# Optimization experiments

Hardware: AMD Instinct MI355X
Metric: run time of the kernel (lower is better)

Reference implementation:

```python
import jax, jax.numpy as jnp
import numpy as np
from jax import lax

V, E, H, MLP, NCLS = 50000, 100, 100, 300, 3
B, T, C = 256, 128, 255


def _lstm_dir(x, Wih, Whh, bih, bhh, reverse):
    # x: [T, B, E]; PyTorch gate order i, f, g, o
    Bsz = x.shape[1]
    h0 = jnp.zeros((Bsz, H), x.dtype)
    c0 = jnp.zeros((Bsz, H), x.dtype)

    def step(carry, xt):
        h, c = carry
        gates = xt @ Wih.T + h @ Whh.T + (bih + bhh)  # [B, 4H]
        i, f, g, o = jnp.split(gates, 4, axis=-1)
        c = jax.nn.sigmoid(f) * c + jax.nn.sigmoid(i) * jnp.tanh(g)
        h = jax.nn.sigmoid(o) * jnp.tanh(c)
        return (h, c), h

    _, hs = lax.scan(step, (h0, c0), x, reverse=reverse)
    return hs  # [T, B, H]


def setup_inputs() -> dict:
    key = jax.random.key(0)
    ks = jax.random.split(key, 16)
    s_e = 1.0 / np.sqrt(H)
    inp = {
        "x": jax.random.randint(ks[0], (B, T), 0, V),
        "paths": jax.random.randint(ks[1], (B, C, 3), 0, T),
        "emb": jax.random.normal(ks[2], (V, E), jnp.float32),
        "Wih_f": jax.random.uniform(ks[3], (4 * H, E), jnp.float32, -s_e, s_e),
        "Whh_f": jax.random.uniform(ks[4], (4 * H, H), jnp.float32, -s_e, s_e),
        "bih_f": jax.random.uniform(ks[5], (4 * H,), jnp.float32, -s_e, s_e),
        "bhh_f": jax.random.uniform(ks[6], (4 * H,), jnp.float32, -s_e, s_e),
        "Wih_b": jax.random.uniform(ks[7], (4 * H, E), jnp.float32, -s_e, s_e),
        "Whh_b": jax.random.uniform(ks[8], (4 * H, H), jnp.float32, -s_e, s_e),
        "bih_b": jax.random.uniform(ks[9], (4 * H,), jnp.float32, -s_e, s_e),
        "bhh_b": jax.random.uniform(ks[10], (4 * H,), jnp.float32, -s_e, s_e),
        "W1": jax.random.normal(ks[11], (6 * H, MLP), jnp.float32) * 0.05,
        "b1": jnp.zeros((MLP,), jnp.float32),
        "W2": jax.random.normal(ks[12], (MLP, NCLS), jnp.float32) * 0.05,
        "b2": jnp.zeros((NCLS,), jnp.float32),
    }
    return inp


def reference(x, paths, emb, Wih_f, Whh_f, bih_f, bhh_f, Wih_b, Whh_b, bih_b, bhh_b, W1, b1, W2, b2):
    # embedding lookup (dropout is eval-mode identity)
    xe = emb[x]                      # [B, T, E]
    xe = jnp.transpose(xe, (1, 0, 2))  # [T, B, E] (seq-major like packed LSTM)
    hf = _lstm_dir(xe, Wih_f, Whh_f, bih_f, bhh_f, reverse=False)
    hb = _lstm_dir(xe, Wih_b, Whh_b, bih_b, bhh_b, reverse=True)
    h = jnp.concatenate([hf, hb], axis=-1)        # [T, B, 2H]
    hbt = jnp.transpose(h, (1, 0, 2))             # [B, T, 2H]
    # gather 3 positions per configuration; index -1 -> zero vector
    idx = jnp.clip(paths, 0, T - 1)               # [B, C, 3]
    g = hbt[jnp.arange(hbt.shape[0])[:, None, None], idx]  # [B, C, 3, 2H]
    g = jnp.where((paths >= 0)[..., None], g, 0.0)
    mlp_in = g.reshape(-1, 6 * H)                 # [B*C, 600]
    hdn = jnp.tanh(mlp_in @ W1 + b1)
    return jax.nn.softmax(hdn @ W2 + b2, axis=-1)  # [B*C, 3]
```

## Files before the change

### kernel.cpp

```cpp
#include <hip/hip_runtime.h>

typedef unsigned short u16;
typedef short short8 __attribute__((ext_vector_type(8)));
typedef float f32x4 __attribute__((ext_vector_type(4)));

__device__ __forceinline__ u16 f2b(float x){
  union{float f; unsigned u;} v; v.f = x;
  unsigned r = (v.u + 0x7FFFu + ((v.u >> 16) & 1u)) >> 16;
  return (u16)r;
}
__device__ __forceinline__ float b2f(u16 h){
  union{unsigned u; float f;} v; v.u = ((unsigned)h) << 16; return v.f;
}
__device__ __forceinline__ float sigm(float x){ return 1.0f/(1.0f + __expf(-x)); }
__device__ __forceinline__ float tanh_f(float x){ return 1.0f - 2.0f/(1.0f + __expf(2.0f*x)); }

__global__ void prep_kernel(const int* __restrict__ x, const float* __restrict__ emb,
   const float* __restrict__ Wih_f, const float* __restrict__ Whh_f,
   const float* __restrict__ bih_f, const float* __restrict__ bhh_f,
   const float* __restrict__ Wih_b, const float* __restrict__ Whh_b,
   const float* __restrict__ bih_b, const float* __restrict__ bhh_b,
   const float* __restrict__ W1,
   u16* __restrict__ xe, u16* __restrict__ wc, float* __restrict__ biasC,
   float* __restrict__ whhT, u16* __restrict__ w1b, u16* __restrict__ hbt)
{
  int id = blockIdx.x*256 + threadIdx.x;
  const int N0 = 32768*128;
  const int N1 = 832*128;
  const int N2 = 800;
  const int N3 = 80000;
  const int N4 = 672*320;
  const int N5 = 32768*24;
  if (id < N0){
    int p = id >> 7, k = id & 127;
    float v = 0.f;
    if (k < 100) v = emb[x[p]*100 + k];
    xe[id] = f2b(v);
    return;
  }
  id -= N0;
  if (id < N1){
    int n = id >> 7, k = id & 127;
    float v = 0.f;
    if (k < 100){
      if (n < 400) v = Wih_f[n*100+k];
      else if (n < 800) v = Wih_b[(n-400)*100+k];
    }
    wc[id] = f2b(v);
    return;
  }
  id -= N1;
  if (id < N2){
    biasC[id] = (id < 400) ? (bih_f[id]+bhh_f[id]) : (bih_b[id-400]+bhh_b[id-400]);
    return;
  }
  id -= N2;
  if (id < N3){
    int d = id / 40000; int rem = id - d*40000; int k = rem / 400; int j = rem - k*400;
    const float* W = d ? Whh_b : Whh_f;
    whhT[id] = W[j*100 + k];
    return;
  }
  id -= N3;
  if (id < N4){
    int k = id / 320; int n = id - k*320;
    int seg = k / 224; int wwk = k - seg*224;
    float v = 0.f;
    if (n < 300 && wwk < 200) v = W1[(seg*200 + wwk)*300 + n];
    w1b[n*672 + k] = f2b(v);
    return;
  }
  id -= N4;
  if (id < N5){
    int p = id / 24; int k = id - p*24;
    hbt[p*224 + 200 + k] = 0;
  }
}

__global__ __launch_bounds__(256) void gemm1_kernel(const u16* __restrict__ xe,
    const u16* __restrict__ wc, const float* __restrict__ biasC, u16* __restrict__ inp)
{
  __shared__ __align__(16) u16 As[64*136];
  __shared__ __align__(16) u16 Bs[64*136];
  const int m0 = blockIdx.x*64, n0 = blockIdx.y*64;
  const int tid = threadIdx.x;
  #pragma unroll
  for (int i=0;i<4;i++){
    int f = i*256 + tid;
    int row = f >> 4, c8 = f & 15;
    *(uint4*)&As[row*136 + c8*8] = *(const uint4*)&xe[(m0+row)*128 + c8*8];
    *(uint4*)&Bs[row*136 + c8*8] = *(const uint4*)&wc[(n0+row)*128 + c8*8];
  }
  __syncthreads();
  const int w = tid >> 6, lane = tid & 63, col = lane & 15, quad = lane >> 4;
  f32x4 acc[4];
  #pragma unroll
  for (int nt=0;nt<4;nt++) acc[nt] = (f32x4){0.f,0.f,0.f,0.f};
  #pragma unroll
  for (int kc=0;kc<4;kc++){
    short8 af = *(const short8*)&As[(w*16+col)*136 + kc*32 + quad*8];
    #pragma unroll
    for (int nt=0;nt<4;nt++){
      short8 bfrag = *(const short8*)&Bs[(nt*16+col)*136 + kc*32 + quad*8];
      acc[nt] = __builtin_amdgcn_mfma_f32_16x16x32_bf16(af, bfrag, acc[nt], 0, 0, 0);
    }
  }
  #pragma unroll
  for (int nt=0;nt<4;nt++){
    int n = n0 + nt*16 + col;
    if (n < 800){
      float bs = biasC[n];
      int dir = (n >= 400) ? 1 : 0;
      int j = n - dir*400;
      #pragma unroll
      for (int r=0;r<4;r++){
        int m = m0 + w*16 + quad*4 + r;
        inp[(dir*32768 + m)*400 + j] = f2b(acc[nt][r] + bs);
      }
    }
  }
}

__global__ __launch_bounds__(448, 4) void lstm_kernel(const u16* __restrict__ inp,
    const float* __restrict__ whhT, u16* __restrict__ hbt)
{
  const int cid = blockIdx.x;
  const int b = cid & 255, dir = cid >> 8;
  const int jj = threadIdx.x;
  __shared__ __align__(16) float hs[104];
  __shared__ float act[400];
  float whh[100];
  if (jj < 400){
    const float* wp = whhT + dir*40000 + jj;
    #pragma unroll
    for (int k=0;k<100;k++) whh[k] = wp[k*400];
  }
  if (jj < 104) hs[jj] = 0.f;
  float c = 0.f;
  const u16* ip = inp + (dir*32768 + b*128)*400;
  u16* hp = hbt + b*128*224;
  __syncthreads();
  for (int step=0; step<128; step++){
    int t = dir ? (127-step) : step;
    if (jj < 400){
      float pre = b2f(ip[t*400 + jj]);
      const float4* h4 = (const float4*)hs;
      float a0=0.f,a1=0.f,a2=0.f,a3=0.f;
      #pragma unroll
      for (int kk=0;kk<25;kk++){
        float4 hv = h4[kk];
        a0 = fmaf(whh[4*kk+0], hv.x, a0);
        a1 = fmaf(whh[4*kk+1], hv.y, a1);
        a2 = fmaf(whh[4*kk+2], hv.z, a2);
        a3 = fmaf(whh[4*kk+3], hv.w, a3);
      }
      float xg = pre + ((a0+a1)+(a2+a3));
      act[jj] = (jj >= 200 && jj < 300) ? tanh_f(xg) : sigm(xg);
    }
    __syncthreads();
    if (jj < 100){
      float ig = act[jj], fg = act[100+jj], gg = act[200+jj], og = act[300+jj];
      c = fg*c + ig*gg;
      float hk = og * tanh_f(c);
      hs[jj] = hk;
      hp[t*224 + dir*100 + jj] = f2b(hk);
    }
    __syncthreads();
  }
}

__global__ __launch_bounds__(512) void mlp_kernel(const u16* __restrict__ hbt,
    const u16* __restrict__ w1b, const int* __restrict__ paths,
    const float* __restrict__ b1, const float* __restrict__ W2,
    const float* __restrict__ b2, float* __restrict__ out)
{
  __shared__ __align__(16) u16 As[128*40];
  __shared__ __align__(16) u16 Bs[320*40];
  const int m0 = blockIdx.x*128;
  const int tid = threadIdx.x;
  const int arow = tid >> 2, ac8 = tid & 3;
  const int am = m0 + arow;
  const int ab = am / 255;
  const int w = tid >> 6, lane = tid & 63, col = lane & 15, quad = lane >> 4;
  f32x4 acc[20];
  #pragma unroll
  for (int nt=0;nt<20;nt++) acc[nt] = (f32x4){0.f,0.f,0.f,0.f};
  for (int kc=0;kc<21;kc++){
    __syncthreads();
    for (int f = tid; f < 1280; f += 512){
      int br = f >> 2, bc = f & 3;
      *(uint4*)&Bs[br*40 + bc*8] = *(const uint4*)&w1b[br*672 + kc*32 + bc*8];
    }
    int seg = (kc >= 14) ? 2 : (kc >= 7 ? 1 : 0);
    int ko = kc - seg*7;
    int it = paths[am*3 + seg];
    uint4 v = make_uint4(0u,0u,0u,0u);
    if (it >= 0){
      int t = it > 127 ? 127 : it;
      v = *(const uint4*)&hbt[(ab*128 + t)*224 + ko*32 + ac8*8];
    }
    *(uint4*)&As[arow*40 + ac8*8] = v;
    __syncthreads();
    short8 af = *(const short8*)&As[(w*16+col)*40 + quad*8];
    #pragma unroll
    for (int nt=0;nt<20;nt++){
      short8 bfrag = *(const short8*)&Bs[(nt*16+col)*40 + quad*8];
      acc[nt] = __builtin_amdgcn_mfma_f32_16x16x32_bf16(af, bfrag, acc[nt], 0, 0, 0);
    }
  }
  float pz[4][3];
  #pragma unroll
  for (int r=0;r<4;r++){ pz[r][0]=0.f; pz[r][1]=0.f; pz[r][2]=0.f; }
  #pragma unroll
  for (int nt=0;nt<20;nt++){
    int n = nt*16 + col;
    if (n < 300){
      float bb = b1[n];
      float w20 = W2[n*3+0], w21 = W2[n*3+1], w22 = W2[n*3+2];
      #pragma unroll
      for (int r=0;r<4;r++){
        float hdn = tanh_f(acc[nt][r] + bb);
        pz[r][0] = fmaf(hdn, w20, pz[r][0]);
        pz[r][1] = fmaf(hdn, w21, pz[r][1]);
        pz[r][2] = fmaf(hdn, w22, pz[r][2]);
      }
    }
  }
  #pragma unroll
  for (int off=1; off<16; off<<=1){
    #pragma unroll
    for (int r=0;r<4;r++){
      pz[r][0] += __shfl_xor(pz[r][0], off, 64);
      pz[r][1] += __shfl_xor(pz[r][1], off, 64);
      pz[r][2] += __shfl_xor(pz[r][2], off, 64);
    }
  }
  float c0 = b2[0], c1 = b2[1], c2 = b2[2];
  #pragma unroll
  for (int r=0;r<4;r++){
    float z0 = pz[r][0]+c0, z1 = pz[r][1]+c1, z2 = pz[r][2]+c2;
    float mx = fmaxf(z0, fmaxf(z1, z2));
    float e0 = __expf(z0-mx), e1 = __expf(z1-mx), e2 = __expf(z2-mx);
    float inv = 1.0f/(e0+e1+e2);
    if (col < 3){
      float pv = (col==0 ? e0 : (col==1 ? e1 : e2)) * inv;
      out[(m0 + w*16 + quad*4 + r)*3 + col] = pv;
    }
  }
}

extern "C" void kernel_launch(void* const* d_in, const int* in_sizes, int n_in,
                              void* d_out, int out_size, void* d_ws, size_t ws_size,
                              hipStream_t stream)
{
  const int*   x     = (const int*)  d_in[0];
  const int*   paths = (const int*)  d_in[1];
  const float* emb   = (const float*)d_in[2];
  const float* Wih_f = (const float*)d_in[3];
  const float* Whh_f = (const float*)d_in[4];
  const float* bih_f = (const float*)d_in[5];
  const float* bhh_f = (const float*)d_in[6];
  const float* Wih_b = (const float*)d_in[7];
  const float* Whh_b = (const float*)d_in[8];
  const float* bih_b = (const float*)d_in[9];
  const float* bhh_b = (const float*)d_in[10];
  const float* W1    = (const float*)d_in[11];
  const float* b1    = (const float*)d_in[12];
  const float* W2    = (const float*)d_in[13];
  const float* b2    = (const float*)d_in[14];
  float* out = (float*)d_out;

  char* ws = (char*)d_ws;
  u16*   xe    = (u16*)  (ws + 0);
  u16*   wc    = (u16*)  (ws + 8388608);
  float* biasC = (float*)(ws + 8601600);
  float* whhT  = (float*)(ws + 8604800);
  u16*   w1b   = (u16*)  (ws + 8924800);
  u16*   inp   = (u16*)  (ws + 9354880);
  u16*   hbt   = (u16*)  (ws + 61783680);

  const int prep_total = 32768*128 + 832*128 + 800 + 80000 + 672*320 + 32768*24;
  prep_kernel<<<(prep_total + 255)/256, 256, 0, stream>>>(
      x, emb, Wih_f, Whh_f, bih_f, bhh_f, Wih_b, Whh_b, bih_b, bhh_b, W1,
      xe, wc, biasC, whhT, w1b, hbt);
  gemm1_kernel<<<dim3(512, 13), 256, 0, stream>>>(xe, wc, biasC, inp);
  lstm_kernel<<<512, 448, 0, stream>>>(inp, whhT, hbt);
  mlp_kernel<<<510, 512, 0, stream>>>(hbt, w1b, paths, b1, W2, b2, out);
}
```

Before: 364.4 us.

## Rewrite LSTM recurrence in inline assembly with interleaved gates and swizzle exchange

Gate columns are permuted so each hidden unit's four gates sit in adjacent lanes, letting the recurrence exchange gate values via ds_swizzle within a quad instead of through shared memory and a second barrier. The step loop is hand-written in inline assembly, with weights held in registers, LDS reads software-pipelined against FMAs, and double-buffered h in LDS so only one barrier per timestep remains. This targets the serial per-step latency of the LSTM, which is likely the dominant kernel. The hand-written asm carries correctness risk from hard-coded registers, exec masks and the waitcnt logic.

Result: slower. 385.2 us (+5.7%).

```diff
diff --git a/kernel.cpp b/kernel.cpp
--- a/kernel.cpp
+++ b/kernel.cpp
@@ -22,7 +22,7 @@
    const float* __restrict__ bih_b, const float* __restrict__ bhh_b,
    const float* __restrict__ W1,
    u16* __restrict__ xe, u16* __restrict__ wc, float* __restrict__ biasC,
-   float* __restrict__ whhT, u16* __restrict__ w1b, u16* __restrict__ hbt)
+   float* __restrict__ whhR, u16* __restrict__ w1b, u16* __restrict__ hbt)
 {
   int id = blockIdx.x*256 + threadIdx.x;
   const int N0 = 32768*128;
@@ -56,9 +56,10 @@
   }
   id -= N2;
   if (id < N3){
-    int d = id / 40000; int rem = id - d*40000; int k = rem / 400; int j = rem - k*400;
+    int d = id / 40000; int rem = id - d*40000; int p = rem / 100; int k = rem - p*100;
+    int uu = p >> 2, gg = p & 3;
     const float* W = d ? Whh_b : Whh_f;
-    whhT[id] = W[j*100 + k];
+    whhR[id] = W[(gg*100 + uu)*100 + k];
     return;
   }
   id -= N3;
@@ -112,60 +113,212 @@
       float bs = biasC[n];
       int dir = (n >= 400) ? 1 : 0;
       int j = n - dir*400;
+      int gg = j / 100, uu = j - gg*100;
+      int pj = uu*4 + gg;
       #pragma unroll
       for (int r=0;r<4;r++){
         int m = m0 + w*16 + quad*4 + r;
-        inp[(dir*32768 + m)*400 + j] = f2b(acc[nt][r] + bs);
+        inp[(dir*32768 + m)*400 + pj] = f2b(acc[nt][r] + bs);
       }
     }
   }
 }
 
-__global__ __launch_bounds__(448, 4) void lstm_kernel(const u16* __restrict__ inp,
-    const float* __restrict__ whhT, u16* __restrict__ hbt)
+#define G4(W0,W1,W2,W3,S0,S1,S2,S3,OFF) \
+  "s_waitcnt lgkmcnt(1)\n\t" \
+  "v_fmac_f32 v8,  v" #W0 ", v" #S0 "\n\t" \
+  "v_fmac_f32 v9,  v" #W1 ", v" #S1 "\n\t" \
+  "v_fmac_f32 v10, v" #W2 ", v" #S2 "\n\t" \
+  "v_fmac_f32 v11, v" #W3 ", v" #S3 "\n\t" \
+  "ds_read_b128 v[" #S0 ":" #S3 "], v12 offset:" #OFF "\n\t"
+#define G4T(W0,W1,W2,W3,S0,S1,S2,S3,CNT) \
+  "s_waitcnt lgkmcnt(" #CNT ")\n\t" \
+  "v_fmac_f32 v8,  v" #W0 ", v" #S0 "\n\t" \
+  "v_fmac_f32 v9,  v" #W1 ", v" #S1 "\n\t" \
+  "v_fmac_f32 v10, v" #W2 ", v" #S2 "\n\t" \
+  "v_fmac_f32 v11, v" #W3 ", v" #S3 "\n\t"
+
+__global__ __launch_bounds__(448) void lstm_kernel(const u16* __restrict__ inp,
+    const float* __restrict__ whhR, u16* __restrict__ hbt)
 {
+  __shared__ __align__(16) float hs2[2][128];
   const int cid = blockIdx.x;
   const int b = cid & 255, dir = cid >> 8;
-  const int jj = threadIdx.x;
-  __shared__ __align__(16) float hs[104];
-  __shared__ float act[400];
-  float whh[100];
-  if (jj < 400){
-    const float* wp = whhT + dir*40000 + jj;
-    #pragma unroll
-    for (int k=0;k<100;k++) whh[k] = wp[k*400];
-  }
-  if (jj < 104) hs[jj] = 0.f;
-  float c = 0.f;
-  const u16* ip = inp + (dir*32768 + b*128)*400;
-  u16* hp = hbt + b*128*224;
+  const int tid = threadIdx.x;
+  for (int i = tid; i < 256; i += 448) ((float*)hs2)[i] = 0.f;
   __syncthreads();
-  for (int step=0; step<128; step++){
-    int t = dir ? (127-step) : step;
-    if (jj < 400){
-      float pre = b2f(ip[t*400 + jj]);
-      const float4* h4 = (const float4*)hs;
-      float a0=0.f,a1=0.f,a2=0.f,a3=0.f;
-      #pragma unroll
-      for (int kk=0;kk<25;kk++){
-        float4 hv = h4[kk];
-        a0 = fmaf(whh[4*kk+0], hv.x, a0);
-        a1 = fmaf(whh[4*kk+1], hv.y, a1);
-        a2 = fmaf(whh[4*kk+2], hv.z, a2);
-        a3 = fmaf(whh[4*kk+3], hv.w, a3);
-      }
-      float xg = pre + ((a0+a1)+(a2+a3));
-      act[jj] = (jj >= 200 && jj < 300) ? tanh_f(xg) : sigm(xg);
-    }
-    __syncthreads();
-    if (jj < 100){
-      float ig = act[jj], fg = act[100+jj], gg = act[200+jj], og = act[300+jj];
-      c = fg*c + ig*gg;
-      float hk = og * tanh_f(c);
-      hs[jj] = hk;
-      hp[t*224 + dir*100 + jj] = f2b(hk);
-    }
-    __syncthreads();
+  if (tid < 400){
+    unsigned long long fe  = __ballot(1);
+    unsigned long long g0e = __ballot((tid & 3) == 0);
+    unsigned long long g1e = __ballot((tid & 3) == 1);
+    unsigned long long g1m = __ballot((tid & 1) != 0);
+    unsigned long long g2m = __ballot((tid & 2) != 0);
+    const int sw  = tid >> 6;
+    const int t0  = dir ? 127 : 0;
+    const int dIb = dir ? -800 : 800;
+    const int dHb = dir ? -448 : 448;
+    const int s4h = 400;
+    const int swb = dir*160000;
+    const unsigned sio = (unsigned)((dir*32768 + b*128 + t0)*400) * 2u;
+    const unsigned sho = (unsigned)((b*128 + t0)*224 + dir*100) * 2u;
+    const unsigned sra = (unsigned)(size_t)&hs2[0][0];
+    const unsigned sha = sra + 512u;
+    asm volatile(
+      "v_mbcnt_lo_u32_b32 v0, -1, 0\n\t"
+      "v_mbcnt_hi_u32_b32 v0, -1, v0\n\t"
+      "v_lshl_add_u32 v0, %[sw], 6, v0\n\t"
+      "v_mul_lo_u32 v1, %[s4h], v0\n\t"
+      "v_add_u32 v1, %[swb], v1\n\t"
+      "v_lshl_add_u32 v15, v0, 1, %[sio]\n\t"
+      "v_lshrrev_b32 v2, 2, v0\n\t"
+      "v_lshl_add_u32 v14, v2, 1, %[sho]\n\t"
+      "v_lshl_add_u32 v13, v2, 2, %[sha]\n\t"
+      "v_mov_b32 v12, %[sra]\n\t"
+      "v_mov_b32 v16, 0\n\t"
+      "s_mov_b32 s20, 128\n\t"
+      "global_load_ushort v17, v15, %[ib]\n\t"
+      "v_add_u32 v15, %[dis], v15\n\t"
+      "global_load_dwordx4 v[24:27],   v1, %[wb]\n\t"
+      "global_load_dwordx4 v[28:31],   v1, %[wb] offset:16\n\t"
+      "global_load_dwordx4 v[32:35],   v1, %[wb] offset:32\n\t"
+      "global_load_dwordx4 v[36:39],   v1, %[wb] offset:48\n\t"
+      "global_load_dwordx4 v[40:43],   v1, %[wb] offset:64\n\t"
+      "global_load_dwordx4 v[44:47],   v1, %[wb] offset:80\n\t"
+      "global_load_dwordx4 v[48:51],   v1, %[wb] offset:96\n\t"
+      "global_load_dwordx4 v[52:55],   v1, %[wb] offset:112\n\t"
+      "global_load_dwordx4 v[56:59],   v1, %[wb] offset:128\n\t"
+      "global_load_dwordx4 v[60:63],   v1, %[wb] offset:144\n\t"
+      "global_load_dwordx4 v[64:67],   v1, %[wb] offset:160\n\t"
+      "global_load_dwordx4 v[68:71],   v1, %[wb] offset:176\n\t"
+      "global_load_dwordx4 v[72:75],   v1, %[wb] offset:192\n\t"
+      "global_load_dwordx4 v[76:79],   v1, %[wb] offset:208\n\t"
+      "global_load_dwordx4 v[80:83],   v1, %[wb] offset:224\n\t"
+      "global_load_dwordx4 v[84:87],   v1, %[wb] offset:240\n\t"
+      "global_load_dwordx4 v[88:91],   v1, %[wb] offset:256\n\t"
+      "global_load_dwordx4 v[92:95],   v1, %[wb] offset:272\n\t"
+      "global_load_dwordx4 v[96:99],   v1, %[wb] offset:288\n\t"
+      "global_load_dwordx4 v[100:103], v1, %[wb] offset:304\n\t"
+      "global_load_dwordx4 v[104:107], v1, %[wb] offset:320\n\t"
+      "global_load_dwordx4 v[108:111], v1, %[wb] offset:336\n\t"
+      "global_load_dwordx4 v[112:115], v1, %[wb] offset:352\n\t"
+      "global_load_dwordx4 v[116:119], v1, %[wb] offset:368\n\t"
+      "global_load_dwordx4 v[120:123], v1, %[wb] offset:384\n\t"
+      "LSTM_T%=:\n\t"
+      "s_waitcnt vmcnt(0)\n\t"
+      "v_lshlrev_b32 v18, 16, v17\n\t"
+      "global_load_ushort v17, v15, %[ib]\n\t"
+      "v_add_u32 v15, %[dis], v15\n\t"
+      "ds_read_b128 v[0:3], v12\n\t"
+      "ds_read_b128 v[4:7], v12 offset:16\n\t"
+      "v_mov_b32 v8, 0\n\t"
+      "v_mov_b32 v9, 0\n\t"
+      "v_mov_b32 v10, 0\n\t"
+      "v_mov_b32 v11, 0\n\t"
+      G4(24,25,26,27,      0,1,2,3,    32)
+      G4(28,29,30,31,      4,5,6,7,    48)
+      G4(32,33,34,35,      0,1,2,3,    64)
+      G4(36,37,38,39,      4,5,6,7,    80)
+      G4(40,41,42,43,      0,1,2,3,    96)
+      G4(44,45,46,47,      4,5,6,7,    112)
+      G4(48,49,50,51,      0,1,2,3,    128)
+      G4(52,53,54,55,      4,5,6,7,    144)
+      G4(56,57,58,59,      0,1,2,3,    160)
+      G4(60,61,62,63,      4,5,6,7,    176)
+      G4(64,65,66,67,      0,1,2,3,    192)
+      G4(68,69,70,71,      4,5,6,7,    208)
+      G4(72,73,74,75,      0,1,2,3,    224)
+      G4(76,77,78,79,      4,5,6,7,    240)
+      G4(80,81,82,83,      0,1,2,3,    256)
+      G4(84,85,86,87,      4,5,6,7,    272)
+      G4(88,89,90,91,      0,1,2,3,    288)
+      G4(92,93,94,95,      4,5,6,7,    304)
+      G4(96,97,98,99,      0,1,2,3,    320)
+      G4(100,101,102,103,  4,5,6,7,    336)
+      G4(104,105,106,107,  0,1,2,3,    352)
+      G4(108,109,110,111,  4,5,6,7,    368)
+      G4(112,113,114,115,  0,1,2,3,    384)
+      G4T(116,117,118,119, 4,5,6,7,    1)
+      G4T(120,121,122,123, 0,1,2,3,    0)
+      "v_add_f32 v8, v8, v9\n\t"
+      "v_add_f32 v10, v10, v11\n\t"
+      "v_add_f32 v8, v8, v10\n\t"
+      "v_add_f32 v18, v8, v18\n\t"
+      "ds_swizzle_b32 v19, v18 offset:0x041f\n\t"
+      "ds_swizzle_b32 v20, v18 offset:0x081f\n\t"
+      "s_waitcnt lgkmcnt(0)\n\t"
+      "ds_swizzle_b32 v21, v19 offset:0x081f\n\t"
+      "s_waitcnt lgkmcnt(0)\n\t"
+      "v_cndmask_b32 v22, v18, v19, %[g1m]\n\t"
+      "v_cndmask_b32 v19, v19, v18, %[g1m]\n\t"
+      "v_cndmask_b32 v23, v20, v21, %[g1m]\n\t"
+      "v_cndmask_b32 v20, v21, v20, %[g1m]\n\t"
+      "v_cndmask_b32 v18, v22, v23, %[g2m]\n\t"
+      "v_cndmask_b32 v21, v23, v22, %[g2m]\n\t"
+      "v_cndmask_b32 v22, v19, v20, %[g2m]\n\t"
+      "v_cndmask_b32 v23, v20, v19, %[g2m]\n\t"
+      "v_mul_f32 v19, 0xbfb8aa3b, v22\n\t"
+      "v_mul_f32 v20, 0xbfb8aa3b, v18\n\t"
+      "v_mul_f32 v22, 0x4038aa3b, v21\n\t"
+      "v_exp_f32 v19, v19\n\t"
+      "v_exp_f32 v20, v20\n\t"
+      "v_exp_f32 v22, v22\n\t"
+      "v_add_f32 v19, 1.0, v19\n\t"
+      "v_add_f32 v20, 1.0, v20\n\t"
+      "v_add_f32 v22, 1.0, v22\n\t"
+      "v_rcp_f32 v19, v19\n\t"
+      "v_rcp_f32 v20, v20\n\t"
+      "v_rcp_f32 v22, v22\n\t"
+      "v_mov_b32 v18, 1.0\n\t"
+      "v_fmac_f32 v18, -2.0, v22\n\t"
+      "v_mul_f32 v20, v20, v18\n\t"
+      "v_fmac_f32 v20, v19, v16\n\t"
+      "v_mov_b32 v16, v20\n\t"
+      "v_mul_f32 v19, 0x4038aa3b, v16\n\t"
+      "v_mul_f32 v21, 0xbfb8aa3b, v23\n\t"
+      "v_exp_f32 v19, v19\n\t"
+      "v_exp_f32 v21, v21\n\t"
+      "v_add_f32 v19, 1.0, v19\n\t"
+      "v_add_f32 v21, 1.0, v21\n\t"
+      "v_rcp_f32 v19, v19\n\t"
+      "v_rcp_f32 v21, v21\n\t"
+      "v_mov_b32 v18, 1.0\n\t"
+      "v_fmac_f32 v18, -2.0, v19\n\t"
+      "v_mul_f32 v20, v21, v18\n\t"
+      "v_cvt_pk_bf16_f32 v22, v20, v20\n\t"
+      "s_mov_b64 exec, %[g0e]\n\t"
+      "ds_write_b32 v13, v20\n\t"
+      "s_mov_b64 exec, %[g1e]\n\t"
+      "global_store_short v14, v22, %[hb]\n\t"
+      "s_mov_b64 exec, %[fe]\n\t"
+      "v_add_u32 v14, %[dhs], v14\n\t"
+      "v_xor_b32 v12, 0x200, v12\n\t"
+      "v_xor_b32 v13, 0x200, v13\n\t"
+      "s_waitcnt lgkmcnt(0)\n\t"
+      "s_barrier\n\t"
+      "s_sub_u32 s20, s20, 1\n\t"
+      "s_cmp_lg_u32 s20, 0\n\t"
+      "s_cbranch_scc1 LSTM_T%=\n\t"
+      :
+      : [sw]"s"(sw), [s4h]"s"(s4h), [swb]"s"(swb),
+        [sio]"s"(sio), [sho]"s"(sho), [sra]"s"(sra), [sha]"s"(sha),
+        [wb]"s"(whhR), [ib]"s"(inp), [hb]"s"(hbt),
+        [dis]"s"(dIb), [dhs]"s"(dHb),
+        [fe]"s"(fe), [g0e]"s"(g0e), [g1e]"s"(g1e), [g1m]"s"(g1m), [g2m]"s"(g2m)
+      : "memory","scc","s20",
+        "v0","v1","v2","v3","v4","v5","v6","v7","v8","v9",
+        "v10","v11","v12","v13","v14","v15","v16","v17","v18","v19",
+        "v20","v21","v22","v23","v24","v25","v26","v27","v28","v29",
+        "v30","v31","v32","v33","v34","v35","v36","v37","v38","v39",
+        "v40","v41","v42","v43","v44","v45","v46","v47","v48","v49",
+        "v50","v51","v52","v53","v54","v55","v56","v57","v58","v59",
+        "v60","v61","v62","v63","v64","v65","v66","v67","v68","v69",
+        "v70","v71","v72","v73","v74","v75","v76","v77","v78","v79",
+        "v80","v81","v82","v83","v84","v85","v86","v87","v88","v89",
+        "v90","v91","v92","v93","v94","v95","v96","v97","v98","v99",
+        "v100","v101","v102","v103","v104","v105","v106","v107","v108","v109",
+        "v110","v111","v112","v113","v114","v115","v116","v117","v118","v119",
+        "v120","v121","v122","v123"
+    );
   }
 }
 
@@ -274,7 +427,7 @@
   u16*   xe    = (u16*)  (ws + 0);
   u16*   wc    = (u16*)  (ws + 8388608);
   float* biasC = (float*)(ws + 8601600);
-  float* whhT  = (float*)(ws + 8604800);
+  float* whhR  = (float*)(ws + 8604800);
   u16*   w1b   = (u16*)  (ws + 8924800);
   u16*   inp   = (u16*)  (ws + 9354880);
   u16*   hbt   = (u16*)  (ws + 61783680);
@@ -282,8 +435,8 @@
   const int prep_total = 32768*128 + 832*128 + 800 + 80000 + 672*320 + 32768*24;
   prep_kernel<<<(prep_total + 255)/256, 256, 0, stream>>>(
       x, emb, Wih_f, Whh_f, bih_f, bhh_f, Wih_b, Whh_b, bih_b, bhh_b, W1,
-      xe, wc, biasC, whhT, w1b, hbt);
+      xe, wc, biasC, whhR, w1b, hbt);
   gemm1_kernel<<<dim3(512, 13), 256, 0, stream>>>(xe, wc, biasC, inp);
-  lstm_kernel<<<512, 448, 0, stream>>>(inp, whhT, hbt);
+  lstm_kernel<<<512, 448, 0, stream>>>(inp, whhR, hbt);
   mlp_kernel<<<510, 512, 0, stream>>>(hbt, w1b, paths, b1, W2, b2, out);
 }
```

## Rewrite LSTM recurrence in inline asm with fp16 dot2 and double-buffered hidden state

Applied to the files above, without the earlier changes.

The LSTM kernel is rewritten in hand-written GCN assembly. Each thread of a quad now handles a quarter of K for four gates of one unit, using packed fp16 v_dot2 on fp16 recurrent weights and DPP quad reductions. The gate nonlinearities and cell update happen in-register, so the per-step act shared array and one of the two barriers per timestep go away. The hidden state is double-buffered in LDS and the next step's pre-activation input is prefetched. Weights and h in fp16 lose precision, and the hardcoded VGPR use and exec-mask tricks are fragile.

New measurement: 373.4 us. 1.02x slower.

```diff
diff --git a/kernel.cpp b/kernel.cpp
--- a/kernel.cpp
+++ b/kernel.cpp
@@ -8,6 +8,9 @@
   union{float f; unsigned u;} v; v.f = x;
   unsigned r = (v.u + 0x7FFFu + ((v.u >> 16) & 1u)) >> 16;
   return (u16)r;
+}
+__device__ __forceinline__ u16 f2h(float x){
+  union{_Float16 h; u16 u;} c; c.h = (_Float16)x; return c.u;
 }
 __device__ __forceinline__ float b2f(u16 h){
   union{unsigned u; float f;} v; v.u = ((unsigned)h) << 16; return v.f;
@@ -22,13 +25,13 @@
    const float* __restrict__ bih_b, const float* __restrict__ bhh_b,
    const float* __restrict__ W1,
    u16* __restrict__ xe, u16* __restrict__ wc, float* __restrict__ biasC,
-   float* __restrict__ whhT, u16* __restrict__ w1b, u16* __restrict__ hbt)
+   u16* __restrict__ whh2, u16* __restrict__ w1b, u16* __restrict__ hbt)
 {
   int id = blockIdx.x*256 + threadIdx.x;
   const int N0 = 32768*128;
   const int N1 = 832*128;
   const int N2 = 800;
-  const int N3 = 80000;
+  const int N3 = 102400;
   const int N4 = 672*320;
   const int N5 = 32768*24;
   if (id < N0){
@@ -56,9 +59,17 @@
   }
   id -= N2;
   if (id < N3){
-    int d = id / 40000; int rem = id - d*40000; int k = rem / 400; int j = rem - k*400;
-    const float* W = d ? Whh_b : Whh_f;
-    whhT[id] = W[j*100 + k];
+    int d = id / 51200; int rem = id - d*51200;
+    int t = rem >> 7;  int e  = rem & 127;
+    int g = e >> 5;    int kq = e & 31;
+    int u = t >> 2;    int q  = t & 3;
+    int k = q*32 + kq;
+    float v = 0.f;
+    if (k < 100){
+      const float* W = d ? Whh_b : Whh_f;
+      v = W[(g*100 + u)*100 + k];
+    }
+    whh2[id] = f2h(v);
     return;
   }
   id -= N3;
@@ -112,60 +123,184 @@
       float bs = biasC[n];
       int dir = (n >= 400) ? 1 : 0;
       int j = n - dir*400;
+      int gg = j / 100, uu = j - gg*100;
+      int pj = uu*4 + gg;
       #pragma unroll
       for (int r=0;r<4;r++){
         int m = m0 + w*16 + quad*4 + r;
-        inp[(dir*32768 + m)*400 + j] = f2b(acc[nt][r] + bs);
+        inp[(dir*32768 + m)*400 + pj] = f2b(acc[nt][r] + bs);
       }
     }
   }
 }
 
-__global__ __launch_bounds__(448, 4) void lstm_kernel(const u16* __restrict__ inp,
-    const float* __restrict__ whhT, u16* __restrict__ hbt)
+#define DSL(CNT, H0,H1,H2,H3, A0,A1,A2,A3, B0,B1,B2,B3, C0,C1,C2,C3, D0,D1,D2,D3) \
+  "s_waitcnt lgkmcnt(" #CNT ")\n\t" \
+  "v_dot2_f32_f16 v16, v" #A0 ", v" #H0 ", v16\n\t" \
+  "v_dot2_f32_f16 v17, v" #B0 ", v" #H0 ", v17\n\t" \
+  "v_dot2_f32_f16 v18, v" #C0 ", v" #H0 ", v18\n\t" \
+  "v_dot2_f32_f16 v19, v" #D0 ", v" #H0 ", v19\n\t" \
+  "v_dot2_f32_f16 v16, v" #A1 ", v" #H1 ", v16\n\t" \
+  "v_dot2_f32_f16 v17, v" #B1 ", v" #H1 ", v17\n\t" \
+  "v_dot2_f32_f16 v18, v" #C1 ", v" #H1 ", v18\n\t" \
+  "v_dot2_f32_f16 v19, v" #D1 ", v" #H1 ", v19\n\t" \
+  "v_dot2_f32_f16 v16, v" #A2 ", v" #H2 ", v16\n\t" \
+  "v_dot2_f32_f16 v17, v" #B2 ", v" #H2 ", v17\n\t" \
+  "v_dot2_f32_f16 v18, v" #C2 ", v" #H2 ", v18\n\t" \
+  "v_dot2_f32_f16 v19, v" #D2 ", v" #H2 ", v19\n\t" \
+  "v_dot2_f32_f16 v16, v" #A3 ", v" #H3 ", v16\n\t" \
+  "v_dot2_f32_f16 v17, v" #B3 ", v" #H3 ", v17\n\t" \
+  "v_dot2_f32_f16 v18, v" #C3 ", v" #H3 ", v18\n\t" \
+  "v_dot2_f32_f16 v19, v" #D3 ", v" #H3 ", v19\n\t"
+
+__global__ __launch_bounds__(448) void lstm_kernel(const u16* __restrict__ inp,
+    const u16* __restrict__ whh2, u16* __restrict__ hbt)
 {
+  __shared__ __align__(512) u16 hs2[256];
   const int cid = blockIdx.x;
   const int b = cid & 255, dir = cid >> 8;
-  const int jj = threadIdx.x;
-  __shared__ __align__(16) float hs[104];
-  __shared__ float act[400];
-  float whh[100];
-  if (jj < 400){
-    const float* wp = whhT + dir*40000 + jj;
-    #pragma unroll
-    for (int k=0;k<100;k++) whh[k] = wp[k*400];
-  }
-  if (jj < 104) hs[jj] = 0.f;
-  float c = 0.f;
-  const u16* ip = inp + (dir*32768 + b*128)*400;
-  u16* hp = hbt + b*128*224;
+  const int tid = threadIdx.x;
+  for (int i = tid; i < 128; i += 448) ((float*)hs2)[i] = 0.f;
   __syncthreads();
-  for (int step=0; step<128; step++){
-    int t = dir ? (127-step) : step;
-    if (jj < 400){
-      float pre = b2f(ip[t*400 + jj]);
-      const float4* h4 = (const float4*)hs;
-      float a0=0.f,a1=0.f,a2=0.f,a3=0.f;
-      #pragma unroll
-      for (int kk=0;kk<25;kk++){
-        float4 hv = h4[kk];
-        a0 = fmaf(whh[4*kk+0], hv.x, a0);
-        a1 = fmaf(whh[4*kk+1], hv.y, a1);
-        a2 = fmaf(whh[4*kk+2], hv.z, a2);
-        a3 = fmaf(whh[4*kk+3], hv.w, a3);
-      }
-      float xg = pre + ((a0+a1)+(a2+a3));
-      act[jj] = (jj >= 200 && jj < 300) ? tanh_f(xg) : sigm(xg);
-    }
-    __syncthreads();
-    if (jj < 100){
-      float ig = act[jj], fg = act[100+jj], gg = act[200+jj], og = act[300+jj];
-      c = fg*c + ig*gg;
-      float hk = og * tanh_f(c);
-      hs[jj] = hk;
-      hp[t*224 + dir*100 + jj] = f2b(hk);
-    }
-    __syncthreads();
+  if (tid < 400){
+    unsigned long long fe  = __ballot(1);
+    unsigned long long g0e = __ballot((tid & 3) == 0);
+    unsigned long long g1e = __ballot((tid & 3) == 1);
+    const int sw  = tid >> 6;
+    const int t0  = dir ? 127 : 0;
+    const int dIb = dir ? -800 : 800;
+    const int dHb = dir ? -448 : 448;
+    const int swb = dir*102400;
+    const unsigned sio = (unsigned)((dir*32768 + b*128 + t0)*400) * 2u;
+    const unsigned sho = (unsigned)((b*128 + t0)*224 + dir*100) * 2u;
+    const unsigned sra = (unsigned)(size_t)&hs2[0];
+    const unsigned sha = sra + 256u;
+    asm volatile(
+      "v_mbcnt_lo_u32_b32 v0, -1, 0\n\t"
+      "v_mbcnt_hi_u32_b32 v0, -1, v0\n\t"
+      "v_lshl_add_u32 v0, %[sw], 6, v0\n\t"
+      "v_lshlrev_b32 v1, 8, v0\n\t"
+      "v_add_u32 v1, %[swb], v1\n\t"
+      "v_lshrrev_b32 v3, 2, v0\n\t"
+      "v_and_b32 v2, 3, v0\n\t"
+      "v_lshl_add_u32 v23, v2, 6, %[sra]\n\t"
+      "v_lshl_add_u32 v24, v3, 1, %[sha]\n\t"
+      "v_lshl_add_u32 v25, v3, 1, %[sho]\n\t"
+      "v_lshl_add_u32 v26, v3, 3, %[sio]\n\t"
+      "v_mov_b32 v22, 0\n\t"
+      "s_mov_b32 s20, 128\n\t"
+      "global_load_dwordx2 v[20:21], v26, %[ib]\n\t"
+      "v_add_u32 v26, %[dis], v26\n\t"
+      "global_load_dwordx4 v[32:35], v1, %[wb]\n\t"
+      "global_load_dwordx4 v[36:39], v1, %[wb] offset:16\n\t"
+      "global_load_dwordx4 v[40:43], v1, %[wb] offset:32\n\t"
+      "global_load_dwordx4 v[44:47], v1, %[wb] offset:48\n\t"
+      "global_load_dwordx4 v[48:51], v1, %[wb] offset:64\n\t"
+      "global_load_dwordx4 v[52:55], v1, %[wb] offset:80\n\t"
+      "global_load_dwordx4 v[56:59], v1, %[wb] offset:96\n\t"
+      "global_load_dwordx4 v[60:63], v1, %[wb] offset:112\n\t"
+      "global_load_dwordx4 v[64:67], v1, %[wb] offset:128\n\t"
+      "global_load_dwordx4 v[68:71], v1, %[wb] offset:144\n\t"
+      "global_load_dwordx4 v[72:75], v1, %[wb] offset:160\n\t"
+      "global_load_dwordx4 v[76:79], v1, %[wb] offset:176\n\t"
+      "global_load_dwordx4 v[80:83], v1, %[wb] offset:192\n\t"
+      "global_load_dwordx4 v[84:87], v1, %[wb] offset:208\n\t"
+      "global_load_dwordx4 v[88:91], v1, %[wb] offset:224\n\t"
+      "global_load_dwordx4 v[92:95], v1, %[wb] offset:240\n\t"
+      "LSTM_T%=:\n\t"
+      "s_waitcnt vmcnt(0)\n\t"
+      "v_lshlrev_b32 v27, 16, v20\n\t"
+      "v_and_b32 v28, 0xffff0000, v20\n\t"
+      "v_lshlrev_b32 v29, 16, v21\n\t"
+      "v_and_b32 v30, 0xffff0000, v21\n\t"
+      "global_load_dwordx2 v[20:21], v26, %[ib]\n\t"
+      "v_add_u32 v26, %[dis], v26\n\t"
+      "ds_read_b128 v[0:3], v23\n\t"
+      "ds_read_b128 v[4:7], v23 offset:16\n\t"
+      "ds_read_b128 v[8:11], v23 offset:32\n\t"
+      "ds_read_b128 v[12:15], v23 offset:48\n\t"
+      "v_mov_b32 v16, 0\n\t"
+      "v_mov_b32 v17, 0\n\t"
+      "v_mov_b32 v18, 0\n\t"
+      "v_mov_b32 v19, 0\n\t"
+      DSL(3, 0,1,2,3,     32,33,34,35, 48,49,50,51, 64,65,66,67, 80,81,82,83)
+      DSL(2, 4,5,6,7,     36,37,38,39, 52,53,54,55, 68,69,70,71, 84,85,86,87)
+      DSL(1, 8,9,10,11,   40,41,42,43, 56,57,58,59, 72,73,74,75, 88,89,90,91)
+      DSL(0, 12,13,14,15, 44,45,46,47, 60,61,62,63, 76,77,78,79, 92,93,94,95)
+      "s_nop 1\n\t"
+      "v_add_f32_dpp v16, v16, v16 quad_perm:[1,0,3,2] row_mask:0xf bank_mask:0xf\n\t"
+      "v_add_f32_dpp v17, v17, v17 quad_perm:[1,0,3,2] row_mask:0xf bank_mask:0xf\n\t"
+      "v_add_f32_dpp v18, v18, v18 quad_perm:[1,0,3,2] row_mask:0xf bank_mask:0xf\n\t"
+      "v_add_f32_dpp v19, v19, v19 quad_perm:[1,0,3,2] row_mask:0xf bank_mask:0xf\n\t"
+      "v_add_f32_dpp v16, v16, v16 quad_perm:[2,3,0,1] row_mask:0xf bank_mask:0xf\n\t"
+      "v_add_f32_dpp v17, v17, v17 quad_perm:[2,3,0,1] row_mask:0xf bank_mask:0xf\n\t"
+      "v_add_f32_dpp v18, v18, v18 quad_perm:[2,3,0,1] row_mask:0xf bank_mask:0xf\n\t"
+      "v_add_f32_dpp v19, v19, v19 quad_perm:[2,3,0,1] row_mask:0xf bank_mask:0xf\n\t"
+      "v_add_f32 v16, v16, v27\n\t"
+      "v_add_f32 v17, v17, v28\n\t"
+      "v_add_f32 v18, v18, v29\n\t"
+      "v_add_f32 v19, v19, v30\n\t"
+      "v_mul_f32 v27, 0xbfb8aa3b, v17\n\t"
+      "v_mul_f32 v28, 0xbfb8aa3b, v16\n\t"
+      "v_mul_f32 v29, 0x4038aa3b, v18\n\t"
+      "v_exp_f32 v27, v27\n\t"
+      "v_exp_f32 v28, v28\n\t"
+      "v_exp_f32 v29, v29\n\t"
+      "v_add_f32 v27, 1.0, v27\n\t"
+      "v_add_f32 v28, 1.0, v28\n\t"
+      "v_add_f32 v29, 1.0, v29\n\t"
+      "v_rcp_f32 v27, v27\n\t"
+      "v_rcp_f32 v28, v28\n\t"
+      "v_rcp_f32 v29, v29\n\t"
+      "v_mov_b32 v30, 1.0\n\t"
+      "v_fmac_f32 v30, -2.0, v29\n\t"
+      "v_mul_f32 v28, v28, v30\n\t"
+      "v_fmac_f32 v28, v27, v22\n\t"
+      "v_mov_b32 v22, v28\n\t"
+      "v_mul_f32 v27, 0x4038aa3b, v22\n\t"
+      "v_mul_f32 v29, 0xbfb8aa3b, v19\n\t"
+      "v_exp_f32 v27, v27\n\t"
+      "v_exp_f32 v29, v29\n\t"
+      "v_add_f32 v27, 1.0, v27\n\t"
+      "v_add_f32 v29, 1.0, v29\n\t"
+      "v_rcp_f32 v27, v27\n\t"
+      "v_rcp_f32 v29, v29\n\t"
+      "v_mov_b32 v30, 1.0\n\t"
+      "v_fmac_f32 v30, -2.0, v27\n\t"
+      "v_mul_f32 v28, v29, v30\n\t"
+      "v_cvt_pk_bf16_f32 v29, v28, v28\n\t"
+      "v_cvt_f16_f32 v27, v28\n\t"
+      "s_mov_b64 exec, %[g0e]\n\t"
+      "ds_write_b16 v24, v27\n\t"
+      "s_mov_b64 exec, %[g1e]\n\t"
+      "global_store_short v25, v29, %[hb]\n\t"
+      "s_mov_b64 exec, %[fe]\n\t"
+      "v_add_u32 v25, %[dhs], v25\n\t"
+      "v_xor_b32 v23, 0x100, v23\n\t"
+      "v_xor_b32 v24, 0x100, v24\n\t"
+      "s_waitcnt lgkmcnt(0)\n\t"
+      "s_barrier\n\t"
+      "s_sub_u32 s20, s20, 1\n\t"
+      "s_cmp_lg_u32 s20, 0\n\t"
+      "s_cbranch_scc1 LSTM_T%=\n\t"
+      :
+      : [sw]"s"(sw), [swb]"s"(swb),
+        [sio]"s"(sio), [sho]"s"(sho), [sra]"s"(sra), [sha]"s"(sha),
+        [wb]"s"(whh2), [ib]"s"(inp), [hb]"s"(hbt),
+        [dis]"s"(dIb), [dhs]"s"(dHb),
+        [fe]"s"(fe), [g0e]"s"(g0e), [g1e]"s"(g1e)
+      : "memory","scc","s20",
+        "v0","v1","v2","v3","v4","v5","v6","v7","v8","v9",
+        "v10","v11","v12","v13","v14","v15","v16","v17","v18","v19",
+        "v20","v21","v22","v23","v24","v25","v26","v27","v28","v29",
+        "v30","v31","v32","v33","v34","v35","v36","v37","v38","v39",
+        "v40","v41","v42","v43","v44","v45","v46","v47","v48","v49",
+        "v50","v51","v52","v53","v54","v55","v56","v57","v58","v59",
+        "v60","v61","v62","v63","v64","v65","v66","v67","v68","v69",
+        "v70","v71","v72","v73","v74","v75","v76","v77","v78","v79",
+        "v80","v81","v82","v83","v84","v85","v86","v87","v88","v89",
+        "v90","v91","v92","v93","v94","v95"
+    );
   }
 }
 
@@ -274,16 +409,16 @@
   u16*   xe    = (u16*)  (ws + 0);
   u16*   wc    = (u16*)  (ws + 8388608);
   float* biasC = (float*)(ws + 8601600);
-  float* whhT  = (float*)(ws + 8604800);
-  u16*   w1b   = (u16*)  (ws + 8924800);
-  u16*   inp   = (u16*)  (ws + 9354880);
-  u16*   hbt   = (u16*)  (ws + 61783680);
-
-  const int prep_total = 32768*128 + 832*128 + 800 + 80000 + 672*320 + 32768*24;
+  u16*   whh2  = (u16*)  (ws + 8604800);
+  u16*   w1b   = (u16*)  (ws + 8809600);
+  u16*   inp   = (u16*)  (ws + 9239680);
+  u16*   hbt   = (u16*)  (ws + 61668480);
+
+  const int prep_total = 32768*128 + 832*128 + 800 + 102400 + 672*320 + 32768*24;
   prep_kernel<<<(prep_total + 255)/256, 256, 0, stream>>>(
       x, emb, Wih_f, Whh_f, bih_f, bhh_f, Wih_b, Whh_b, bih_b, bhh_b, W1,
-      xe, wc, biasC, whhT, w1b, hbt);
+      xe, wc, biasC, whh2, w1b, hbt);
   gemm1_kernel<<<dim3(512, 13), 256, 0, stream>>>(xe, wc, biasC, inp);
-  lstm_kernel<<<512, 448, 0, stream>>>(inp, whhT, hbt);
+  lstm_kernel<<<512, 448, 0, stream>>>(inp, whh2, hbt);
   mlp_kernel<<<510, 512, 0, stream>>>(hbt, w1b, paths, b1, W2, b2, out);
 }
```
